# Kernel tuning notes

Hardware: AMD Instinct MI355X
Metric: run time of the kernel (lower is better)

## Reference

```python
import jax, jax.numpy as jnp
import numpy as np
from jax import lax

BN_EPS = 1e-5


def _conv(x, w, b, stride):
    # x: [N,C,H,W], w: [O,I,3,3], stride 2, padding 1
    y = lax.conv_general_dilated(
        x, w, window_strides=(stride, stride), padding=((1, 1), (1, 1)),
        dimension_numbers=('NCHW', 'OIHW', 'NCHW'))
    return y + b[None, :, None, None]


def _batchnorm(x, gamma, beta):
    # training-mode BN: batch statistics over (N,H,W)
    mean = jnp.mean(x, axis=(0, 2, 3), keepdims=True)
    var = jnp.var(x, axis=(0, 2, 3), keepdims=True)
    xn = (x - mean) * lax.rsqrt(var + BN_EPS)
    return xn * gamma[None, :, None, None] + beta[None, :, None, None]


def _maxpool2(x):
    return lax.reduce_window(x, -jnp.inf, lax.max, (1, 1, 2, 2), (1, 1, 2, 2), 'VALID')


def setup_inputs() -> dict:
    key = jax.random.key(0)
    ks = jax.random.split(key, 8)
    B, C, H, W = 128, 3, 224, 224
    x = jax.random.normal(ks[0], (B, C, H, W), dtype=jnp.float32)
    conv1_w = jax.random.normal(ks[1], (16, 3, 3, 3), dtype=jnp.float32) * (1.0 / np.sqrt(3 * 9))
    conv1_b = jnp.zeros((16,), dtype=jnp.float32)
    bn1_g = jnp.ones((16,), dtype=jnp.float32)
    bn1_b = jnp.zeros((16,), dtype=jnp.float32)
    conv2_w = jax.random.normal(ks[2], (32, 16, 3, 3), dtype=jnp.float32) * (1.0 / np.sqrt(16 * 9))
    conv2_b = jnp.zeros((32,), dtype=jnp.float32)
    bn2_g = jnp.ones((32,), dtype=jnp.float32)
    bn2_b = jnp.zeros((32,), dtype=jnp.float32)
    fc_w = jax.random.normal(ks[3], (1, 32), dtype=jnp.float32) * (1.0 / np.sqrt(32))
    fc_b = jnp.zeros((1,), dtype=jnp.float32)
    return dict(x=x, conv1_w=conv1_w, conv1_b=conv1_b, bn1_g=bn1_g, bn1_b=bn1_b,
                conv2_w=conv2_w, conv2_b=conv2_b, bn2_g=bn2_g, bn2_b=bn2_b,
                fc_w=fc_w, fc_b=fc_b)


def reference(x, conv1_w, conv1_b, bn1_g, bn1_b, conv2_w, conv2_b, bn2_g, bn2_b, fc_w, fc_b):
    h = jax.nn.relu(_batchnorm(_conv(x, conv1_w, conv1_b, 2), bn1_g, bn1_b))   # [B,16,112,112]
    h = _maxpool2(h)                                                           # [B,16,56,56]
    h = jax.nn.relu(_batchnorm(_conv(h, conv2_w, conv2_b, 2), bn2_g, bn2_b))   # [B,32,28,28]
    h = jnp.mean(h, axis=(2, 3))                                               # AdaptiveAvgPool2d((1,1)) -> [B,32]
    logits = h @ fc_w.T + fc_b                                                 # [B,1]
    # Quantum circuit: RY(theta) on all wires, CNOT chain, <Z_0>.
    # Z on the control wire commutes with every CNOT -> expval = cos(theta).
    probs = jnp.cos(logits)                                                    # [B,1]
    return jnp.concatenate((probs, 1.0 - probs), axis=-1)                      # [B,2]
```

## Files before the change

kernel.cpp:

```cpp
#include <hip/hip_runtime.h>
#include <math.h>

#define BATCH 128
#define CIN 3
#define H 224
#define W 224
#define C1 16
#define HP 56
#define WP 56
#define C2 32
#define H2 28
#define W2 28

__global__ __launch_bounds__(256) void conv1_fused_k(
    const float* __restrict__ x, const float* __restrict__ w1,
    const float* __restrict__ b1, float2* __restrict__ mm,
    float* __restrict__ s_sum, float* __restrict__ s_sq)
{
    __shared__ float red[4][8], redq[4][8];
    const int tid = threadIdx.x;
    const int t = blockIdx.x * 256 + tid;
    const int c0 = blockIdx.y * 8;
    const int n = t / 1568;
    const int r = t % 1568;
    const int phh = r / 56;
    const int pw  = r % 56;
    const int rbase = 8 * phh - 1;
    const int cbase = 4 * pw;
    const bool topok = phh > 0;
    const bool pwok  = pw > 0;

    float accA[8][4], accB[8][4];
#pragma unroll
    for (int j = 0; j < 8; ++j) {
        const float bb = b1[c0 + j];
#pragma unroll
        for (int q = 0; q < 4; ++q) { accA[j][q] = bb; accB[j][q] = bb; }
    }

#pragma unroll
    for (int ci = 0; ci < CIN; ++ci) {
        const float* img = x + (n * CIN + ci) * (H * W);
        float p[9][5];
#pragma unroll
        for (int l = 0; l < 9; ++l) {
            const int ih = max(rbase + l, 0);
            const float* rowp = img + ih * W;
            const float4 f4 = *(const float4*)(rowp + cbase);
            const float lf = rowp[max(cbase - 1, 0)];
            const bool rok = (l > 0) || topok;
            p[l][0] = (rok && pwok) ? lf : 0.0f;
            p[l][1] = rok ? f4.x : 0.0f;
            p[l][2] = rok ? f4.y : 0.0f;
            p[l][3] = rok ? f4.z : 0.0f;
            p[l][4] = rok ? f4.w : 0.0f;
        }
#pragma unroll
        for (int j = 0; j < 8; ++j) {
            const float* wc = w1 + ((c0 + j) * CIN + ci) * 9;
#pragma unroll
            for (int kh = 0; kh < 3; ++kh) {
#pragma unroll
                for (int kw = 0; kw < 3; ++kw) {
                    const float wv = wc[kh * 3 + kw];
                    accA[j][0] += wv * p[kh][kw];
                    accA[j][1] += wv * p[kh][kw + 2];
                    accA[j][2] += wv * p[kh + 2][kw];
                    accA[j][3] += wv * p[kh + 2][kw + 2];
                    accB[j][0] += wv * p[4 + kh][kw];
                    accB[j][1] += wv * p[4 + kh][kw + 2];
                    accB[j][2] += wv * p[6 + kh][kw];
                    accB[j][3] += wv * p[6 + kh][kw + 2];
                }
            }
        }
    }

#pragma unroll
    for (int j = 0; j < 8; ++j) {
        const int o = (n * C1 + c0 + j) * (HP * WP) + (2 * phh) * WP + pw;
        const float a0 = accA[j][0], a1 = accA[j][1], a2 = accA[j][2], a3 = accA[j][3];
        const float b0 = accB[j][0], b1v = accB[j][1], b2v = accB[j][2], b3 = accB[j][3];
        mm[o] = make_float2(fmaxf(fmaxf(a0, a1), fmaxf(a2, a3)),
                            fminf(fminf(a0, a1), fminf(a2, a3)));
        mm[o + WP] = make_float2(fmaxf(fmaxf(b0, b1v), fmaxf(b2v, b3)),
                                 fminf(fminf(b0, b1v), fminf(b2v, b3)));
        float s = a0 + a1 + a2 + a3 + b0 + b1v + b2v + b3;
        float q = a0 * a0 + a1 * a1 + a2 * a2 + a3 * a3
                + b0 * b0 + b1v * b1v + b2v * b2v + b3 * b3;
#pragma unroll
        for (int off = 32; off > 0; off >>= 1) {
            s += __shfl_xor(s, off);
            q += __shfl_xor(q, off);
        }
        if ((tid & 63) == 0) { red[tid >> 6][j] = s; redq[tid >> 6][j] = q; }
    }
    __syncthreads();
    if (tid < 8) {
        atomicAdd(&s_sum[c0 + tid],
                  red[0][tid] + red[1][tid] + red[2][tid] + red[3][tid]);
    } else if (tid < 16) {
        const int j = tid - 8;
        atomicAdd(&s_sq[c0 + j],
                  redq[0][j] + redq[1][j] + redq[2][j] + redq[3][j]);
    }
}

__global__ __launch_bounds__(256) void conv2_k(
    const float2* __restrict__ mm,
    const float* __restrict__ s1sum, const float* __restrict__ s1sq,
    const float* __restrict__ g1, const float* __restrict__ be1,
    const float* __restrict__ w2, const float* __restrict__ b2,
    float* __restrict__ y2,
    float* __restrict__ s_sum, float* __restrict__ s_sq)
{
    __shared__ float red[4][8], redq[4][8];
    const int tid = threadIdx.x;
    const int t = blockIdx.x * 256 + tid;
    const int c0 = blockIdx.y * 8;
    const int n = t / 784;
    const int p = t % 784;
    const int oh = p / W2, ow = p % W2;
    const bool topok = oh > 0;
    const bool owok  = ow > 0;
    const float inv1 = 1.0f / (float)(BATCH * 112 * 112);

    float acc[8];
#pragma unroll
    for (int c = 0; c < 8; ++c) acc[c] = b2[c0 + c];

#pragma unroll 2
    for (int ci = 0; ci < C1; ++ci) {
        const float mean = s1sum[ci] * inv1;
        const float var  = s1sq[ci] * inv1 - mean * mean;
        const float s1 = g1[ci] * rsqrtf(var + 1e-5f);
        const float t1 = be1[ci] - mean * s1;

        const float2* pl = mm + (n * C1 + ci) * (HP * WP);
        float v[3][3];
#pragma unroll
        for (int kh = 0; kh < 3; ++kh) {
            const int ih = max(2 * oh - 1 + kh, 0);
            const float2* rowp = pl + ih * WP;
            const float4 f4 = *(const float4*)(rowp + 2 * ow);
            const float2 lp = rowp[max(2 * ow - 1, 0)];
            const bool rok = (kh > 0) || topok;
            const float h0 = fmaxf(0.0f, fmaxf(s1 * lp.x + t1, s1 * lp.y + t1));
            const float h1 = fmaxf(0.0f, fmaxf(s1 * f4.x + t1, s1 * f4.y + t1));
            const float h2 = fmaxf(0.0f, fmaxf(s1 * f4.z + t1, s1 * f4.w + t1));
            v[kh][0] = (rok && owok) ? h0 : 0.0f;
            v[kh][1] = rok ? h1 : 0.0f;
            v[kh][2] = rok ? h2 : 0.0f;
        }
#pragma unroll
        for (int c = 0; c < 8; ++c) {
            const float* wc = w2 + ((c0 + c) * C1 + ci) * 9;
            float a = acc[c];
            a += wc[0] * v[0][0]; a += wc[1] * v[0][1]; a += wc[2] * v[0][2];
            a += wc[3] * v[1][0]; a += wc[4] * v[1][1]; a += wc[5] * v[1][2];
            a += wc[6] * v[2][0]; a += wc[7] * v[2][1]; a += wc[8] * v[2][2];
            acc[c] = a;
        }
    }

#pragma unroll
    for (int c = 0; c < 8; ++c) {
        const float a = acc[c];
        y2[(n * C2 + c0 + c) * (H2 * W2) + p] = a;
        float s = a, q = a * a;
#pragma unroll
        for (int off = 32; off > 0; off >>= 1) {
            s += __shfl_xor(s, off);
            q += __shfl_xor(q, off);
        }
        if ((tid & 63) == 0) { red[tid >> 6][c] = s; redq[tid >> 6][c] = q; }
    }
    __syncthreads();
    if (tid < 8) {
        atomicAdd(&s_sum[c0 + tid],
                  red[0][tid] + red[1][tid] + red[2][tid] + red[3][tid]);
    } else if (tid < 16) {
        const int c = tid - 8;
        atomicAdd(&s_sq[c0 + c],
                  redq[0][c] + redq[1][c] + redq[2][c] + redq[3][c]);
    }
}

__global__ __launch_bounds__(256) void head_fused_k(
    const float* __restrict__ y2,
    const float* __restrict__ s2sum, const float* __restrict__ s2sq,
    const float* __restrict__ g2, const float* __restrict__ be2,
    const float* __restrict__ fcw, const float* __restrict__ fcb,
    float* __restrict__ out)
{
    __shared__ float feat[C2];
    const int n = blockIdx.x;
    const int tid = threadIdx.x;
    const int wave = tid >> 6, lane = tid & 63;
    const float inv2 = 1.0f / (float)(BATCH * H2 * W2);
#pragma unroll
    for (int k = 0; k < 8; ++k) {
        const int c = wave * 8 + k;
        const float mean = s2sum[c] * inv2;
        const float var  = s2sq[c] * inv2 - mean * mean;
        const float s = g2[c] * rsqrtf(var + 1e-5f);
        const float t = be2[c] - mean * s;
        const float4* yp = (const float4*)(y2 + (n * C2 + c) * (H2 * W2));
        float a = 0.0f;
        for (int i = lane; i < 196; i += 64) {
            const float4 v = yp[i];
            a += fmaxf(0.0f, s * v.x + t) + fmaxf(0.0f, s * v.y + t)
               + fmaxf(0.0f, s * v.z + t) + fmaxf(0.0f, s * v.w + t);
        }
#pragma unroll
        for (int off = 32; off > 0; off >>= 1) a += __shfl_xor(a, off);
        if (lane == 0) feat[c] = a * (1.0f / (H2 * W2));
    }
    __syncthreads();
    if (tid == 0) {
        float logit = fcb[0];
#pragma unroll
        for (int c = 0; c < C2; ++c) logit += feat[c] * fcw[c];
        const float pc = cosf(logit);
        out[2 * n]     = pc;
        out[2 * n + 1] = 1.0f - pc;
    }
}

extern "C" void kernel_launch(void* const* d_in, const int* in_sizes, int n_in,
                              void* d_out, int out_size, void* d_ws, size_t ws_size,
                              hipStream_t stream) {
    const float* x   = (const float*)d_in[0];
    const float* w1  = (const float*)d_in[1];
    const float* b1  = (const float*)d_in[2];
    const float* g1  = (const float*)d_in[3];
    const float* be1 = (const float*)d_in[4];
    const float* w2  = (const float*)d_in[5];
    const float* b2  = (const float*)d_in[6];
    const float* g2  = (const float*)d_in[7];
    const float* be2 = (const float*)d_in[8];
    const float* fcw = (const float*)d_in[9];
    const float* fcb = (const float*)d_in[10];
    float* out = (float*)d_out;

    float* ws = (float*)d_ws;
    float2* mm = (float2*)ws;
    float* y2 = ws + (size_t)2 * BATCH * C1 * HP * WP;
    float* stats = y2 + (size_t)BATCH * C2 * H2 * W2;
    float* s1sum = stats;
    float* s1sq  = stats + 16;
    float* s2sum = stats + 32;
    float* s2sq  = stats + 64;

    hipMemsetAsync(stats, 0, 96 * sizeof(float), stream);

    conv1_fused_k<<<dim3(784, 2), 256, 0, stream>>>(x, w1, b1, mm, s1sum, s1sq);
    conv2_k<<<dim3(392, 4), 256, 0, stream>>>(mm, s1sum, s1sq, g1, be1,
                                              w2, b2, y2, s2sum, s2sq);
    head_fused_k<<<BATCH, 256, 0, stream>>>(y2, s2sum, s2sq, g2, be2,
                                            fcw, fcb, out);
}
```

Measured before the change: 215.3 us.

## Halve conv1 per-thread work and double-buffer input loads in both convs

Conv1 threads now compute a single pooled output row instead of two, which doubles the grid and cuts registers per thread. Both conv kernels add software prefetching: the raw input rows for the next input channel are loaded into a register double buffer while the current channel is computed, and conv2's channel loop is fully unrolled. The aim is better latency hiding through more waves and overlapped loads. The cost is that conv1 re-reads the overlapping halo row between adjacent pooled rows, and the extra prefetch registers may lower occupancy.

Measured after the change: 282.3 us. 31.1% more time.

```diff
diff --git a/kernel.cpp b/kernel.cpp
--- a/kernel.cpp
+++ b/kernel.cpp
@@ -12,6 +12,19 @@
 #define H2 28
 #define W2 28
 
+__device__ __forceinline__ void c1_loadraw(const float* __restrict__ img,
+                                           int rbase, int cbase,
+                                           float4 f4[5], float lf[5])
+{
+#pragma unroll
+    for (int r = 0; r < 5; ++r) {
+        const int ih = max(rbase + r, 0);
+        const float* rowp = img + ih * W;
+        f4[r] = *(const float4*)(rowp + cbase);
+        lf[r] = rowp[max(cbase - 1, 0)];
+    }
+}
+
 __global__ __launch_bounds__(256) void conv1_fused_k(
     const float* __restrict__ x, const float* __restrict__ w1,
     const float* __restrict__ b1, float2* __restrict__ mm,
@@ -21,39 +34,41 @@
     const int tid = threadIdx.x;
     const int t = blockIdx.x * 256 + tid;
     const int c0 = blockIdx.y * 8;
-    const int n = t / 1568;
-    const int r = t % 1568;
-    const int phh = r / 56;
-    const int pw  = r % 56;
-    const int rbase = 8 * phh - 1;
+    const int n = t / 3136;
+    const int p = t % 3136;
+    const int ph = p / WP, pw = p % WP;
+    const int rbase = 4 * ph - 1;
     const int cbase = 4 * pw;
-    const bool topok = phh > 0;
+    const bool topok = ph > 0;
     const bool pwok  = pw > 0;
 
-    float accA[8][4], accB[8][4];
+    float acc[8][4];
 #pragma unroll
     for (int j = 0; j < 8; ++j) {
         const float bb = b1[c0 + j];
 #pragma unroll
-        for (int q = 0; q < 4; ++q) { accA[j][q] = bb; accB[j][q] = bb; }
-    }
+        for (int q = 0; q < 4; ++q) acc[j][q] = bb;
+    }
+
+    float4 rf4[2][5];
+    float  rlf[2][5];
+    c1_loadraw(x + (n * CIN + 0) * (H * W), rbase, cbase, rf4[0], rlf[0]);
 
 #pragma unroll
     for (int ci = 0; ci < CIN; ++ci) {
-        const float* img = x + (n * CIN + ci) * (H * W);
-        float p[9][5];
-#pragma unroll
-        for (int l = 0; l < 9; ++l) {
-            const int ih = max(rbase + l, 0);
-            const float* rowp = img + ih * W;
-            const float4 f4 = *(const float4*)(rowp + cbase);
-            const float lf = rowp[max(cbase - 1, 0)];
-            const bool rok = (l > 0) || topok;
-            p[l][0] = (rok && pwok) ? lf : 0.0f;
-            p[l][1] = rok ? f4.x : 0.0f;
-            p[l][2] = rok ? f4.y : 0.0f;
-            p[l][3] = rok ? f4.z : 0.0f;
-            p[l][4] = rok ? f4.w : 0.0f;
+        if (ci + 1 < CIN)
+            c1_loadraw(x + (n * CIN + ci + 1) * (H * W), rbase, cbase,
+                       rf4[(ci + 1) & 1], rlf[(ci + 1) & 1]);
+        float P[5][5];
+#pragma unroll
+        for (int r = 0; r < 5; ++r) {
+            const float4 f4 = rf4[ci & 1][r];
+            const bool rok = (r > 0) || topok;
+            P[r][0] = (rok && pwok) ? rlf[ci & 1][r] : 0.0f;
+            P[r][1] = rok ? f4.x : 0.0f;
+            P[r][2] = rok ? f4.y : 0.0f;
+            P[r][3] = rok ? f4.z : 0.0f;
+            P[r][4] = rok ? f4.w : 0.0f;
         }
 #pragma unroll
         for (int j = 0; j < 8; ++j) {
@@ -63,14 +78,10 @@
 #pragma unroll
                 for (int kw = 0; kw < 3; ++kw) {
                     const float wv = wc[kh * 3 + kw];
-                    accA[j][0] += wv * p[kh][kw];
-                    accA[j][1] += wv * p[kh][kw + 2];
-                    accA[j][2] += wv * p[kh + 2][kw];
-                    accA[j][3] += wv * p[kh + 2][kw + 2];
-                    accB[j][0] += wv * p[4 + kh][kw];
-                    accB[j][1] += wv * p[4 + kh][kw + 2];
-                    accB[j][2] += wv * p[6 + kh][kw];
-                    accB[j][3] += wv * p[6 + kh][kw + 2];
+                    acc[j][0] += wv * P[kh][kw];
+                    acc[j][1] += wv * P[kh][kw + 2];
+                    acc[j][2] += wv * P[kh + 2][kw];
+                    acc[j][3] += wv * P[kh + 2][kw + 2];
                 }
             }
         }
@@ -78,16 +89,13 @@
 
 #pragma unroll
     for (int j = 0; j < 8; ++j) {
-        const int o = (n * C1 + c0 + j) * (HP * WP) + (2 * phh) * WP + pw;
-        const float a0 = accA[j][0], a1 = accA[j][1], a2 = accA[j][2], a3 = accA[j][3];
-        const float b0 = accB[j][0], b1v = accB[j][1], b2v = accB[j][2], b3 = accB[j][3];
-        mm[o] = make_float2(fmaxf(fmaxf(a0, a1), fmaxf(a2, a3)),
-                            fminf(fminf(a0, a1), fminf(a2, a3)));
-        mm[o + WP] = make_float2(fmaxf(fmaxf(b0, b1v), fmaxf(b2v, b3)),
-                                 fminf(fminf(b0, b1v), fminf(b2v, b3)));
-        float s = a0 + a1 + a2 + a3 + b0 + b1v + b2v + b3;
-        float q = a0 * a0 + a1 * a1 + a2 * a2 + a3 * a3
-                + b0 * b0 + b1v * b1v + b2v * b2v + b3 * b3;
+        const float a0 = acc[j][0], a1 = acc[j][1];
+        const float a2 = acc[j][2], a3 = acc[j][3];
+        mm[(n * C1 + c0 + j) * (HP * WP) + p] =
+            make_float2(fmaxf(fmaxf(a0, a1), fmaxf(a2, a3)),
+                        fminf(fminf(a0, a1), fminf(a2, a3)));
+        float s = a0 + a1 + a2 + a3;
+        float q = a0 * a0 + a1 * a1 + a2 * a2 + a3 * a3;
 #pragma unroll
         for (int off = 32; off > 0; off >>= 1) {
             s += __shfl_xor(s, off);
@@ -103,6 +111,19 @@
         const int j = tid - 8;
         atomicAdd(&s_sq[c0 + j],
                   redq[0][j] + redq[1][j] + redq[2][j] + redq[3][j]);
+    }
+}
+
+__device__ __forceinline__ void c2_loadraw(const float2* __restrict__ pl,
+                                           int oh, int ow,
+                                           float4 f4[3], float2 f2[3])
+{
+#pragma unroll
+    for (int kh = 0; kh < 3; ++kh) {
+        const int ih = max(2 * oh - 1 + kh, 0);
+        const float2* rowp = pl + ih * WP;
+        f4[kh] = *(const float4*)(rowp + 2 * ow);
+        f2[kh] = rowp[max(2 * ow - 1, 0)];
     }
 }
 
@@ -129,21 +150,26 @@
 #pragma unroll
     for (int c = 0; c < 8; ++c) acc[c] = b2[c0 + c];
 
-#pragma unroll 2
+    float4 qf4[2][3];
+    float2 qf2[2][3];
+    c2_loadraw(mm + (n * C1 + 0) * (HP * WP), oh, ow, qf4[0], qf2[0]);
+
+#pragma unroll
     for (int ci = 0; ci < C1; ++ci) {
+        if (ci + 1 < C1)
+            c2_loadraw(mm + (n * C1 + ci + 1) * (HP * WP), oh, ow,
+                       qf4[(ci + 1) & 1], qf2[(ci + 1) & 1]);
+
         const float mean = s1sum[ci] * inv1;
         const float var  = s1sq[ci] * inv1 - mean * mean;
         const float s1 = g1[ci] * rsqrtf(var + 1e-5f);
         const float t1 = be1[ci] - mean * s1;
 
-        const float2* pl = mm + (n * C1 + ci) * (HP * WP);
         float v[3][3];
 #pragma unroll
         for (int kh = 0; kh < 3; ++kh) {
-            const int ih = max(2 * oh - 1 + kh, 0);
-            const float2* rowp = pl + ih * WP;
-            const float4 f4 = *(const float4*)(rowp + 2 * ow);
-            const float2 lp = rowp[max(2 * ow - 1, 0)];
+            const float4 f4 = qf4[ci & 1][kh];
+            const float2 lp = qf2[ci & 1][kh];
             const bool rok = (kh > 0) || topok;
             const float h0 = fmaxf(0.0f, fmaxf(s1 * lp.x + t1, s1 * lp.y + t1));
             const float h1 = fmaxf(0.0f, fmaxf(s1 * f4.x + t1, s1 * f4.y + t1));
@@ -254,7 +280,7 @@
 
     hipMemsetAsync(stats, 0, 96 * sizeof(float), stream);
 
-    conv1_fused_k<<<dim3(784, 2), 256, 0, stream>>>(x, w1, b1, mm, s1sum, s1sq);
+    conv1_fused_k<<<dim3(1568, 2), 256, 0, stream>>>(x, w1, b1, mm, s1sum, s1sq);
     conv2_k<<<dim3(392, 4), 256, 0, stream>>>(mm, s1sum, s1sq, g1, be1,
                                               w2, b2, y2, s2sum, s2sq);
     head_fused_k<<<BATCH, 256, 0, stream>>>(y2, s2sum, s2sq, g2, be2,
```
